# Kernel tuning notes

Hardware: AMD Instinct MI355X
Metric: run time of the kernel (lower is better)

Reference implementation:

```python
import jax, jax.numpy as jnp
import numpy as np

B, N, D, K = 4, 4096, 2048, 4  # batch, seq_len, hidden_size, conv_kernel


def setup_inputs() -> dict:
    key = jax.random.key(0)
    k1, k2, k3 = jax.random.split(key, 3)
    x = jax.random.normal(k1, (B, N, D), dtype=jnp.float32)
    conv_weight = jax.random.normal(k2, (D, K), dtype=jnp.float32) * 0.1  # depthwise weight [D, K]
    conv_bias = jax.random.normal(k3, (D,), dtype=jnp.float32) * 0.1
    return {"x": x, "conv_weight": conv_weight, "conv_bias": conv_bias}


def reference(x, conv_weight, conv_bias):
    # Prefill path of TTTConv: depthwise causal conv1d + cache-state extraction.
    Bx, Nx, Dx = x.shape
    Kx = conv_weight.shape[1]
    xt = jnp.transpose(x, (0, 2, 1))  # [B, D, N]
    kernel = conv_weight[:, None, :]  # [D, 1, K] (O, I/groups, K)
    y = jax.lax.conv_general_dilated(
        xt, kernel,
        window_strides=(1,),
        padding=[(Kx - 1, 0)],  # causal left pad only (causal_conv1d_fn semantics)
        dimension_numbers=("NCH", "OIH", "NCH"),
        feature_group_count=Dx,
    )
    y = y + conv_bias[None, :, None]
    conv_output = jnp.transpose(y, (0, 2, 1))  # [B, N, D]
    # cache state: F.pad(x^T, (K - N, 0)) with N >= K crops to the last K timesteps
    conv_states = xt[:, :, Nx - Kx:]  # [B, D, K]
    return conv_output, conv_states
```

## Files before the change

### kernel.cpp

```cpp
#include <hip/hip_runtime.h>


constexpr int B = 4, N = 4096, D = 2048, K = 4;
constexpr int T = 8;
constexpr int BLK = 256;
constexpr int DV = D / 4;
constexpr int DBLKS = DV / BLK;
constexpr int NCHUNKS = N / T;

__global__ __launch_bounds__(BLK) void tttconv_main(
    const float* __restrict__ x, const float* __restrict__ w,
    const float* __restrict__ bias, float* __restrict__ out)
{
    int bid = blockIdx.x;
    int b = bid / (NCHUNKS * DBLKS);
    int rem = bid % (NCHUNKS * DBLKS);
    int nchunk = rem / DBLKS;
    int dblk = rem % DBLKS;
    int dv = dblk * BLK + threadIdx.x;
    int d = dv * 4;
    int n0 = nchunk * T;

    const float4* w4 = (const float4*)(w + (size_t)d * K);
    float4 wr0 = w4[0];
    float4 wr1 = w4[1];
    float4 wr2 = w4[2];
    float4 wr3 = w4[3];
    float4 bv = *(const float4*)(bias + d);

    const float* xbase = x + ((size_t)b * N) * D + d;
    float4 xin[T + K - 1];
    if (n0 >= K - 1) {
        #pragma unroll
        for (int j = 0; j < T + K - 1; ++j)
            xin[j] = *(const float4*)(xbase + (size_t)(n0 - (K - 1) + j) * D);
    } else {
        #pragma unroll
        for (int j = 0; j < T + K - 1; ++j) {
            int n = n0 - (K - 1) + j;
            xin[j] = (n >= 0) ? *(const float4*)(xbase + (size_t)n * D)
                              : make_float4(0.f, 0.f, 0.f, 0.f);
        }
    }

    float* obase = out + ((size_t)b * N) * D + d;
    #pragma unroll
    for (int t = 0; t < T; ++t) {
        float4 acc = bv;
        acc.x += wr0.x * xin[t + 0].x + wr0.y * xin[t + 1].x + wr0.z * xin[t + 2].x + wr0.w * xin[t + 3].x;
        acc.y += wr1.x * xin[t + 0].y + wr1.y * xin[t + 1].y + wr1.z * xin[t + 2].y + wr1.w * xin[t + 3].y;
        acc.z += wr2.x * xin[t + 0].z + wr2.y * xin[t + 1].z + wr2.z * xin[t + 2].z + wr2.w * xin[t + 3].z;
        acc.w += wr3.x * xin[t + 0].w + wr3.y * xin[t + 1].w + wr3.z * xin[t + 2].w + wr3.w * xin[t + 3].w;
        *(float4*)(obase + (size_t)(n0 + t) * D) = acc;
    }
}

__global__ void tttconv_states(const float* __restrict__ x, float* __restrict__ st)
{
    int idx = blockIdx.x * blockDim.x + threadIdx.x;
    if (idx >= B * D * K) return;
    int k = idx % K;
    int d = (idx / K) % D;
    int b = idx / (K * D);
    st[idx] = x[((size_t)b * N + (N - K + k)) * D + d];
}

extern "C" void kernel_launch(void* const* d_in, const int* in_sizes, int n_in,
                              void* d_out, int out_size, void* d_ws, size_t ws_size,
                              hipStream_t stream)
{
    const float* x    = (const float*)d_in[0];
    const float* w    = (const float*)d_in[1];
    const float* bias = (const float*)d_in[2];
    float* out = (float*)d_out;

    tttconv_main<<<B * NCHUNKS * DBLKS, BLK, 0, stream>>>(x, w, bias, out);

    float* st = out + (size_t)B * N * D;
    tttconv_states<<<(B * D * K + 255) / 256, 256, 0, stream>>>(x, st);
}
```

Baseline: 230.5 us.

## Fuse state extraction, remap blocks per XCD, nontemporal stores, larger time tile

Folds the conv-state extraction into the main kernel so the last time chunk writes the final K timesteps from registers, which drops the second launch. Block IDs are remapped so contiguous work lands on the same XCD for L2 locality. Output stores become nontemporal to avoid polluting cache. The time tile doubles to 16 to cut halo reloads, at the cost of more registers per thread and fewer workgroups.

After: 238.1 us. 3.3% more time.

```diff
diff --git a/kernel.cpp b/kernel.cpp
--- a/kernel.cpp
+++ b/kernel.cpp
@@ -2,19 +2,32 @@
 
 
 constexpr int B = 4, N = 4096, D = 2048, K = 4;
-constexpr int T = 8;
+constexpr int T = 16;
 constexpr int BLK = 256;
 constexpr int DV = D / 4;
 constexpr int DBLKS = DV / BLK;
 constexpr int NCHUNKS = N / T;
+constexpr int NWG = B * NCHUNKS * DBLKS;
+constexpr int NXCD = 8;
+constexpr int CPX = NWG / NXCD;
+
+typedef float v4f __attribute__((ext_vector_type(4)));
+
+__device__ inline void nt_store4(float* p, float4 v) {
+    v4f t = {v.x, v.y, v.z, v.w};
+    __builtin_nontemporal_store(t, (v4f*)p);
+}
 
 __global__ __launch_bounds__(BLK) void tttconv_main(
     const float* __restrict__ x, const float* __restrict__ w,
-    const float* __restrict__ bias, float* __restrict__ out)
+    const float* __restrict__ bias, float* __restrict__ out,
+    float* __restrict__ st)
 {
     int bid = blockIdx.x;
-    int b = bid / (NCHUNKS * DBLKS);
-    int rem = bid % (NCHUNKS * DBLKS);
+    int lid = (bid % NXCD) * CPX + (bid / NXCD);
+
+    int b = lid / (NCHUNKS * DBLKS);
+    int rem = lid % (NCHUNKS * DBLKS);
     int nchunk = rem / DBLKS;
     int dblk = rem % DBLKS;
     int dv = dblk * BLK + threadIdx.x;
@@ -51,18 +64,20 @@
         acc.y += wr1.x * xin[t + 0].y + wr1.y * xin[t + 1].y + wr1.z * xin[t + 2].y + wr1.w * xin[t + 3].y;
         acc.z += wr2.x * xin[t + 0].z + wr2.y * xin[t + 1].z + wr2.z * xin[t + 2].z + wr2.w * xin[t + 3].z;
         acc.w += wr3.x * xin[t + 0].w + wr3.y * xin[t + 1].w + wr3.z * xin[t + 2].w + wr3.w * xin[t + 3].w;
-        *(float4*)(obase + (size_t)(n0 + t) * D) = acc;
+        nt_store4(obase + (size_t)(n0 + t) * D, acc);
     }
-}
 
-__global__ void tttconv_states(const float* __restrict__ x, float* __restrict__ st)
-{
-    int idx = blockIdx.x * blockDim.x + threadIdx.x;
-    if (idx >= B * D * K) return;
-    int k = idx % K;
-    int d = (idx / K) % D;
-    int b = idx / (K * D);
-    st[idx] = x[((size_t)b * N + (N - K + k)) * D + d];
+    if (nchunk == NCHUNKS - 1) {
+        float* sbase = st + ((size_t)b * D + d) * K;
+        float4 s0 = make_float4(xin[T - 1].x, xin[T].x, xin[T + 1].x, xin[T + 2].x);
+        float4 s1 = make_float4(xin[T - 1].y, xin[T].y, xin[T + 1].y, xin[T + 2].y);
+        float4 s2 = make_float4(xin[T - 1].z, xin[T].z, xin[T + 1].z, xin[T + 2].z);
+        float4 s3 = make_float4(xin[T - 1].w, xin[T].w, xin[T + 1].w, xin[T + 2].w);
+        *(float4*)(sbase + 0 * K) = s0;
+        *(float4*)(sbase + 1 * K) = s1;
+        *(float4*)(sbase + 2 * K) = s2;
+        *(float4*)(sbase + 3 * K) = s3;
+    }
 }
 
 extern "C" void kernel_launch(void* const* d_in, const int* in_sizes, int n_in,
@@ -73,9 +88,7 @@
     const float* w    = (const float*)d_in[1];
     const float* bias = (const float*)d_in[2];
     float* out = (float*)d_out;
+    float* st  = out + (size_t)B * N * D;
 
-    tttconv_main<<<B * NCHUNKS * DBLKS, BLK, 0, stream>>>(x, w, bias, out);
-
-    float* st = out + (size_t)B * N * D;
-    tttconv_states<<<(B * D * K + 255) / 256, 256, 0, stream>>>(x, st);
+    tttconv_main<<<NWG, BLK, 0, stream>>>(x, w, bias, out, st);
 }
```
